# Performance work log

Hardware: AMD Instinct MI355X
Metric: run time of the kernel (lower is better)

Reference implementation:

```python
import jax, jax.numpy as jnp
import numpy as np
import math

B, T, C = 2, 2048, 1024
H = 16
HD = C // H  # 64
LAMBDA_INIT = 0.7 - 0.6 * math.exp(-0.3 * (2 - 1))
EPS = 1e-5


def setup_inputs() -> dict:
    key = jax.random.key(0)
    ks = jax.random.split(key, 12)
    s = 1.0 / math.sqrt(C)
    return {
        'x':   jax.random.normal(ks[0], (B, T, C), jnp.float32),
        'Wq1': jax.random.normal(ks[1], (C, C), jnp.float32) * s,
        'Wq2': jax.random.normal(ks[2], (C, C), jnp.float32) * s,
        'Wk1': jax.random.normal(ks[3], (C, C), jnp.float32) * s,
        'Wk2': jax.random.normal(ks[4], (C, C), jnp.float32) * s,
        'Wv':  jax.random.normal(ks[5], (2 * C, C), jnp.float32) * s,
        'Wc':  jax.random.normal(ks[6], (C, 2 * C), jnp.float32) * (1.0 / math.sqrt(2 * C)),
        'lq1': jax.random.normal(ks[7], (H, HD), jnp.float32) * 0.1,
        'lk1': jax.random.normal(ks[8], (H, HD), jnp.float32) * 0.1,
        'lq2': jax.random.normal(ks[9], (H, HD), jnp.float32) * 0.1,
        'lk2': jax.random.normal(ks[10], (H, HD), jnp.float32) * 0.1,
    }


def _heads(x, W, d):
    # x:[B,T,C] @ W.T:[C,out] -> [B,H,T,d]
    b, t, _ = x.shape
    return jnp.einsum('btc,dc->btd', x, W).reshape(b, t, H, d).transpose(0, 2, 1, 3)


def reference(x, Wq1, Wq2, Wk1, Wk2, Wv, Wc, lq1, lk1, lq2, lk2):
    b, t, c = x.shape
    q1 = _heads(x, Wq1, HD)
    q2 = _heads(x, Wq2, HD)
    k1 = _heads(x, Wk1, HD)
    k2 = _heads(x, Wk2, HD)
    v = _heads(x, Wv, 2 * HD)  # [B,H,T,2hd]
    scale = 1.0 / math.sqrt(HD)
    causal = jnp.tril(jnp.ones((t, t), bool))  # [T,T]
    neg = jnp.float32(-jnp.inf)
    att1 = jnp.einsum('bhqd,bhkd->bhqk', q1, k1) * scale
    att2 = jnp.einsum('bhqd,bhkd->bhqk', q2, k2) * scale
    att1 = jax.nn.softmax(jnp.where(causal, att1, neg), axis=-1)
    att2 = jax.nn.softmax(jnp.where(causal, att2, neg), axis=-1)
    lam1 = jnp.exp(jnp.sum(lq1 * lk1, -1))  # [H]
    lam2 = jnp.exp(jnp.sum(lq2 * lk2, -1))
    lam_full = (lam1 - lam2 + LAMBDA_INIT)[None, :, None, None]
    att = att1 - lam_full * att2
    y = jnp.einsum('bhqk,bhkd->bhqd', att, v)  # [B,H,T,2hd]
    # sub-layernorm over last dim, no affine
    mu = jnp.mean(y, -1, keepdims=True)
    var = jnp.mean(jnp.square(y - mu), -1, keepdims=True)
    y = (y - mu) * jax.lax.rsqrt(var + EPS)
    y = y * (1.0 - LAMBDA_INIT)
    y = y.transpose(0, 2, 1, 3).reshape(b, t, 2 * c)
    return jnp.einsum('btd,cd->btc', y, Wc)
```

## Files before the change

### kernel.cpp

```cpp
#include <hip/hip_runtime.h>
#include <stdint.h>

typedef unsigned short u16;
typedef unsigned int   u32;
typedef short  short8  __attribute__((ext_vector_type(8)));
typedef float  f32x4   __attribute__((ext_vector_type(4)));
typedef u16    u16x4   __attribute__((ext_vector_type(4)));
typedef u32    u32x4   __attribute__((ext_vector_type(4)));

#define LAMBDA_INIT   0.25550906759096927f
#define ONE_MINUS_LI  0.7444909324090307f
#define QSCALE        0.18033688011112043f

__device__ __forceinline__ u16 f2bf(float f) {
  union { float f; u32 u; } v; v.f = f;
  u32 r = v.u + 0x7fffu + ((v.u >> 16) & 1u);
  return (u16)(r >> 16);
}

__device__ __forceinline__ u32 packtr(float a, float b) {
  return (__builtin_bit_cast(u32, a) >> 16) | (__builtin_bit_cast(u32, b) & 0xffff0000u);
}

__device__ __forceinline__ float expv(float x) {
  float r; asm("v_exp_f32 %0, %1" : "=v"(r) : "v"(x)); return r;
}

__device__ __forceinline__ void gload16(const void* g, void* l) {
  __builtin_amdgcn_global_load_lds(
      (const __attribute__((address_space(1))) void*)g,
      (__attribute__((address_space(3))) void*)l, 16, 0, 0);
}

__global__ __launch_bounds__(256) void k_cvt12(
    const float* __restrict__ x,  const float* __restrict__ wq1,
    const float* __restrict__ wq2, const float* __restrict__ wk1,
    const float* __restrict__ wk2, const float* __restrict__ wv,
    const float* __restrict__ wc,
    u16* __restrict__ xb, u16* __restrict__ wall, u16* __restrict__ wcb) {
  const int seg = blockIdx.y;
  const float* s;
  u16* d;
  if (seg < 4)       { s = x + (size_t)seg * 1048576;        d = xb + (size_t)seg * 1048576; }
  else if (seg == 4) { s = wq1;                              d = wall; }
  else if (seg == 5) { s = wq2;                              d = wall + 1048576; }
  else if (seg == 6) { s = wk1;                              d = wall + 2097152; }
  else if (seg == 7) { s = wk2;                              d = wall + 3145728; }
  else if (seg < 10) { s = wv + (size_t)(seg - 8) * 1048576; d = wall + 4194304 + (size_t)(seg - 8) * 1048576; }
  else               { s = wc + (size_t)(seg - 10) * 1048576; d = wcb + (size_t)(seg - 10) * 1048576; }
  int i = (blockIdx.x * 256 + threadIdx.x) * 4;
  float4 v = *(const float4*)(s + i);
  u16x4 o = { f2bf(v.x), f2bf(v.y), f2bf(v.z), f2bf(v.w) };
  *(u16x4*)(d + i) = o;
}

__device__ __forceinline__ void gemm_tile_128(
    const u16* __restrict__ A, const u16* __restrict__ Bm, int K,
    int m0, int n0, char* smem, f32x4 acc[4][4]) {
  const int tid = threadIdx.x;
  const int l = tid & 63, w = tid >> 6, g = l >> 4, q = l & 15;
  const int wm = w >> 1, wn = w & 1;
  char* As = smem;
  char* Bs = smem + 16384;
#pragma unroll
  for (int mi = 0; mi < 4; mi++)
#pragma unroll
    for (int ni = 0; ni < 4; ni++) acc[mi][ni] = (f32x4){0.f, 0.f, 0.f, 0.f};

  const int nkt = K >> 6;
  for (int kt = 0; kt < nkt; ++kt) {
    __syncthreads();
#pragma unroll
    for (int i = 0; i < 4; i++) {
      int cc = i * 256 + tid;
      int row = cc >> 3, off = cc & 7;
      int sw = (off * 16) ^ ((row & 7) << 4);
      gload16((const char*)A + ((size_t)(m0 + row) * K + kt * 64) * 2 + sw, As + cc * 16);
      gload16((const char*)Bm + ((size_t)(n0 + row) * K + kt * 64) * 2 + sw, Bs + cc * 16);
    }
    __syncthreads();
#pragma unroll
    for (int ks = 0; ks < 2; ++ks) {
      short8 af[4], bf[4];
#pragma unroll
      for (int mi = 0; mi < 4; mi++) {
        int row = wm * 64 + mi * 16 + q;
        af[mi] = *(const short8*)(As + ((row * 128 + ks * 64 + g * 16) ^ ((row & 7) << 4)));
      }
#pragma unroll
      for (int ni = 0; ni < 4; ni++) {
        int row = wn * 64 + ni * 16 + q;
        bf[ni] = *(const short8*)(Bs + ((row * 128 + ks * 64 + g * 16) ^ ((row & 7) << 4)));
      }
#pragma unroll
      for (int mi = 0; mi < 4; mi++)
#pragma unroll
        for (int ni = 0; ni < 4; ni++)
          acc[mi][ni] = __builtin_amdgcn_mfma_f32_16x16x32_bf16(af[mi], bf[ni], acc[mi][ni], 0, 0, 0);
    }
  }
}

__global__ __launch_bounds__(256) void k_gemm_qkv(
    const u16* __restrict__ xb, const u16* __restrict__ wall,
    u16* __restrict__ q1, u16* __restrict__ q2,
    u16* __restrict__ k1, u16* __restrict__ k2,
    u16* __restrict__ vt) {
  __shared__ __align__(16) char smem[32768];
  f32x4 acc[4][4];
  const int n0 = blockIdx.x * 128, m0 = blockIdx.y * 128;
  gemm_tile_128(xb, wall, 1024, m0, n0, smem, acc);

  const int l = threadIdx.x & 63, w = threadIdx.x >> 6, g = l >> 4, q = l & 15;
  const int wm = w >> 1, wn = w & 1;
  const int seg = n0 >> 10;
  const float sc = (seg < 2) ? QSCALE : 1.0f;
  u16* qk = (seg == 0) ? q1 : (seg == 1) ? q2 : (seg == 2) ? k1 : k2;
#pragma unroll
  for (int mi = 0; mi < 4; mi++)
#pragma unroll
    for (int ni = 0; ni < 4; ni++) {
      int row0 = m0 + wm * 64 + mi * 16 + 4 * g;
      int col = n0 + wn * 64 + ni * 16 + q;
      int bb = row0 >> 11;
      if (seg < 4) {
        int h = (col >> 6) & 15, hd = col & 63;
#pragma unroll
        for (int r = 0; r < 4; r++) {
          int t = (row0 + r) & 2047;
          qk[(((size_t)bb * 16 + h) * 2048 + t) * 64 + hd] = f2bf(acc[mi][ni][r] * sc);
        }
      } else {
        int nv = col - 4096, hh = nv >> 7, d = nv & 127;
        int t = row0 & 2047;
        u16x4 pv;
#pragma unroll
        for (int r = 0; r < 4; r++) pv[r] = f2bf(acc[mi][ni][r]);
        size_t addr = (size_t)(bb * 16 + hh) * 262144 + (size_t)(t >> 6) * 8192
                    + (size_t)(((((t >> 5) & 1) * 8 + (d >> 4)) * 512)
                               + ((t >> 3) & 3) * 128 + (d & 15) * 8 + (t & 7));
        *(u16x4*)(vt + addr) = pv;
      }
    }
}

__global__ __launch_bounds__(256) void k_attn(
    const u16* __restrict__ q1p, const u16* __restrict__ q2p,
    const u16* __restrict__ k1p, const u16* __restrict__ k2p,
    const u16* __restrict__ vfp,
    const float* __restrict__ lq1, const float* __restrict__ lk1,
    const float* __restrict__ lq2, const float* __restrict__ lk2,
    u16* __restrict__ ybp) {
  __shared__ __align__(16) char smem[32768];
  const int fid = blockIdx.x;
  const int xcd = fid & 7;
  const int p = (fid >> 3) & 31;
  const int k = fid >> 8;
  const int t8 = p >> 2;
  const int tile = (k == 0) ? (31 - t8) : (k == 1) ? t8
                 : (k == 2) ? (23 - t8) : (8 + t8);
  const int bh = xcd * 4 + (p & 3);
  const int b = bh >> 4, h = bh & 15;
  const int tid = threadIdx.x, w = tid >> 6, l = tid & 63, g = l >> 4, q = l & 15;
  const int nchunk = 2 * tile + 2;
  const int qrow = tile * 64 + w * 16 + q;

  float a1 = lq1[h * 64 + l] * lk1[h * 64 + l];
  float a2 = lq2[h * 64 + l] * lk2[h * 64 + l];
#pragma unroll
  for (int off = 32; off; off >>= 1) {
    a1 += __shfl_xor(a1, off);
    a2 += __shfl_xor(a2, off);
  }
  const float lam = expf(a1) - expf(a2) + LAMBDA_INIT;

  short8 qf[2][2];
  {
    size_t qoff = ((size_t)bh * 2048 + qrow) * 64;
#pragma unroll
    for (int ks = 0; ks < 2; ++ks) {
      qf[0][ks] = *(const short8*)(q1p + qoff + ks * 32 + g * 8);
      qf[1][ks] = *(const short8*)(q2p + qoff + ks * 32 + g * 8);
    }
  }
  f32x4 o[2][8];
  float lsum[2] = {0.f, 0.f};
#pragma unroll
  for (int s = 0; s < 2; s++)
#pragma unroll
    for (int mt = 0; mt < 8; mt++) o[s][mt] = (f32x4){0.f, 0.f, 0.f, 0.f};

  auto stage_kv = [&](char* sb, int kv0) {
    int kv = tid >> 3, off = tid & 7;
    int sw = (off * 16) ^ ((kv & 7) << 4);
    size_t rb = ((size_t)bh * 2048 + kv0 + kv) * 128;
    gload16((const char*)k1p + rb + sw, sb + tid * 16);
    gload16((const char*)k2p + rb + sw, sb + 4096 + tid * 16);
    const char* vsrc = (const char*)vfp + (size_t)bh * 524288
                     + (size_t)(kv0 >> 6) * 16384 + (size_t)((kv0 >> 5) & 1) * 8192;
    gload16(vsrc + tid * 16, sb + 8192 + tid * 16);
    gload16(vsrc + 4096 + tid * 16, sb + 12288 + tid * 16);
  };

  stage_kv(smem, 0);

  for (int i = 0; i < nchunk; ++i) {
    char* sb = smem + (i & 1) * 16384;
    asm volatile("s_waitcnt vmcnt(0)" ::: "memory");
    __builtin_amdgcn_s_barrier();
    if (i + 1 < nchunk) stage_kv(smem + ((i + 1) & 1) * 16384, (i + 1) * 32);

    const int kv0 = i * 32;
    const bool diag = (i >= nchunk - 2);

    u32 pk[2][4];
#pragma unroll
    for (int s = 0; s < 2; ++s) {
      const char* Ks = sb + s * 4096;
      f32x4 s0 = {0.f, 0.f, 0.f, 0.f}, s1 = {0.f, 0.f, 0.f, 0.f};
#pragma unroll
      for (int ks = 0; ks < 2; ++ks) {
        short8 af0 = *(const short8*)(Ks + ((q * 128 + ks * 64 + g * 16) ^ ((q & 7) << 4)));
        short8 af1 = *(const short8*)(Ks + (((16 + q) * 128 + ks * 64 + g * 16) ^ ((q & 7) << 4)));
        s0 = __builtin_amdgcn_mfma_f32_16x16x32_bf16(af0, qf[s][ks], s0, 0, 0, 0);
        s1 = __builtin_amdgcn_mfma_f32_16x16x32_bf16(af1, qf[s][ks], s1, 0, 0, 0);
      }
      const int kb0 = kv0 + 4 * g, kb1 = kb0 + 16;
      if (diag) {
#pragma unroll
        for (int r = 0; r < 4; r++) {
          s0[r] = (kb0 + r > qrow) ? -1e30f : s0[r];
          s1[r] = (kb1 + r > qrow) ? -1e30f : s1[r];
        }
      }
      float p0[4], p1[4], rs = 0.f;
#pragma unroll
      for (int r = 0; r < 4; r++) {
        p0[r] = expv(s0[r]);
        p1[r] = expv(s1[r]);
        rs += p0[r] + p1[r];
      }
      lsum[s] += rs;

      u32 pk0[2] = { packtr(p0[0], p0[1]), packtr(p0[2], p0[3]) };
      u32 pk1[2] = { packtr(p1[0], p1[1]), packtr(p1[2], p1[3]) };
      int srcA = q + (g & 1) * 32;
      int srcB = srcA + 16;
      u32 xa0 = (u32)__shfl((int)pk0[0], srcA), xa1 = (u32)__shfl((int)pk0[1], srcA);
      u32 xa2 = (u32)__shfl((int)pk0[0], srcB), xa3 = (u32)__shfl((int)pk0[1], srcB);
      u32 xb0 = (u32)__shfl((int)pk1[0], srcA), xb1 = (u32)__shfl((int)pk1[1], srcA);
      u32 xb2 = (u32)__shfl((int)pk1[0], srcB), xb3 = (u32)__shfl((int)pk1[1], srcB);
      bool lo = (g < 2);
      pk[s][0] = lo ? xa0 : xb0;
      pk[s][1] = lo ? xa1 : xb1;
      pk[s][2] = lo ? xa2 : xb2;
      pk[s][3] = lo ? xa3 : xb3;
    }
    u32x4 t0 = {pk[0][0], pk[0][1], pk[0][2], pk[0][3]};
    u32x4 t1 = {pk[1][0], pk[1][1], pk[1][2], pk[1][3]};
    short8 pf0 = __builtin_bit_cast(short8, t0);
    short8 pf1 = __builtin_bit_cast(short8, t1);
    const char* Vb = sb + 8192 + l * 16;
    __builtin_amdgcn_s_setprio(1);
#pragma unroll
    for (int mt = 0; mt < 8; ++mt) {
      short8 vf = *(const short8*)(Vb + mt * 1024);
      o[0][mt] = __builtin_amdgcn_mfma_f32_16x16x32_bf16(vf, pf0, o[0][mt], 0, 0, 0);
      o[1][mt] = __builtin_amdgcn_mfma_f32_16x16x32_bf16(vf, pf1, o[1][mt], 0, 0, 0);
    }
    __builtin_amdgcn_s_setprio(0);
  }

  float l0 = lsum[0]; l0 += __shfl_xor(l0, 16); l0 += __shfl_xor(l0, 32);
  float l1 = lsum[1]; l1 += __shfl_xor(l1, 16); l1 += __shfl_xor(l1, 32);
  const float inv0 = 1.f / l0, inv1 = 1.f / l1;
  float sum = 0.f, ssq = 0.f;
#pragma unroll
  for (int mt = 0; mt < 8; ++mt)
#pragma unroll
    for (int r = 0; r < 4; r++) {
      float y = o[0][mt][r] * inv0 - lam * (o[1][mt][r] * inv1);
      o[0][mt][r] = y;
      sum += y;
      ssq += y * y;
    }
  sum += __shfl_xor(sum, 16); sum += __shfl_xor(sum, 32);
  ssq += __shfl_xor(ssq, 16); ssq += __shfl_xor(ssq, 32);
  const float mean = sum * (1.f / 128.f);
  const float var = ssq * (1.f / 128.f) - mean * mean;
  const float rstd = rsqrtf(var + 1e-5f) * ONE_MINUS_LI;
  u16* dst = ybp + ((size_t)(b * 2048 + qrow)) * 2048 + h * 128;
#pragma unroll
  for (int mt = 0; mt < 8; ++mt) {
    u16x4 pv;
#pragma unroll
    for (int r = 0; r < 4; r++) pv[r] = f2bf((o[0][mt][r] - mean) * rstd);
    *(u16x4*)(dst + mt * 16 + 4 * g) = pv;
  }
}

__global__ __launch_bounds__(512) void k_gemm_out(
    const u16* __restrict__ yb, const u16* __restrict__ wcb,
    float* __restrict__ out) {
  __shared__ __align__(16) char smem[32768];
  const int tid = threadIdx.x;
  const int l = tid & 63, w = tid >> 6, g = l >> 4, q = l & 15;
  const int wm = w >> 1, wn = w & 1;
  const int n0 = blockIdx.x * 128, m0 = blockIdx.y * 128;
  char* As = smem;
  char* Bs = smem + 16384;
  f32x4 acc[2][4];
#pragma unroll
  for (int mi = 0; mi < 2; mi++)
#pragma unroll
    for (int ni = 0; ni < 4; ni++) acc[mi][ni] = (f32x4){0.f, 0.f, 0.f, 0.f};

  for (int kt = 0; kt < 32; ++kt) {
    __syncthreads();
#pragma unroll
    for (int i = 0; i < 2; i++) {
      int cc = i * 512 + tid;
      int row = cc >> 3, off = cc & 7;
      int sw = (off * 16) ^ ((row & 7) << 4);
      gload16((const char*)yb + ((size_t)(m0 + row) * 2048 + kt * 64) * 2 + sw, As + cc * 16);
      gload16((const char*)wcb + ((size_t)(n0 + row) * 2048 + kt * 64) * 2 + sw, Bs + cc * 16);
    }
    __syncthreads();
#pragma unroll
    for (int ks = 0; ks < 2; ++ks) {
      short8 af[2], bf[4];
#pragma unroll
      for (int mi = 0; mi < 2; mi++) {
        int row = wm * 32 + mi * 16 + q;
        af[mi] = *(const short8*)(As + ((row * 128 + ks * 64 + g * 16) ^ ((row & 7) << 4)));
      }
#pragma unroll
      for (int ni = 0; ni < 4; ni++) {
        int row = wn * 64 + ni * 16 + q;
        bf[ni] = *(const short8*)(Bs + ((row * 128 + ks * 64 + g * 16) ^ ((row & 7) << 4)));
      }
#pragma unroll
      for (int mi = 0; mi < 2; mi++)
#pragma unroll
        for (int ni = 0; ni < 4; ni++)
          acc[mi][ni] = __builtin_amdgcn_mfma_f32_16x16x32_bf16(af[mi], bf[ni], acc[mi][ni], 0, 0, 0);
    }
  }
#pragma unroll
  for (int mi = 0; mi < 2; mi++)
#pragma unroll
    for (int ni = 0; ni < 4; ni++)
#pragma unroll
      for (int r = 0; r < 4; r++) {
        int row = m0 + wm * 32 + mi * 16 + 4 * g + r;
        int col = n0 + wn * 64 + ni * 16 + q;
        out[(size_t)row * 1024 + col] = acc[mi][ni][r];
      }
}

extern "C" void kernel_launch(void* const* d_in, const int* in_sizes, int n_in,
                              void* d_out, int out_size, void* d_ws, size_t ws_size,
                              hipStream_t stream) {
  const float* x   = (const float*)d_in[0];
  const float* Wq1 = (const float*)d_in[1];
  const float* Wq2 = (const float*)d_in[2];
  const float* Wk1 = (const float*)d_in[3];
  const float* Wk2 = (const float*)d_in[4];
  const float* Wv  = (const float*)d_in[5];
  const float* Wc  = (const float*)d_in[6];
  const float* lq1 = (const float*)d_in[7];
  const float* lk1 = (const float*)d_in[8];
  const float* lq2 = (const float*)d_in[9];
  const float* lk2 = (const float*)d_in[10];

  char* ws = (char*)d_ws;
  u16* xb   = (u16*)(ws);
  u16* wall = (u16*)(ws + 8388608);
  u16* wcb  = (u16*)(ws + 20971520);
  u16* q1   = (u16*)(ws + 25165824);
  u16* q2   = (u16*)(ws + 33554432);
  u16* k1   = (u16*)(ws + 41943040);
  u16* k2   = (u16*)(ws + 50331648);
  u16* vt   = (u16*)(ws + 58720256);
  u16* yb   = (u16*)(ws + 75497472);

  k_cvt12<<<dim3(1024, 12), 256, 0, stream>>>(x, Wq1, Wq2, Wk1, Wk2, Wv, Wc,
                                              xb, wall, wcb);
  k_gemm_qkv<<<dim3(48, 32), 256, 0, stream>>>(xb, wall, q1, q2, k1, k2, vt);
  k_attn<<<1024, 256, 0, stream>>>(q1, q2, k1, k2, vt,
                                   lq1, lk1, lq2, lk2, yb);
  k_gemm_out<<<dim3(8, 32), 512, 0, stream>>>(yb, wcb, (float*)d_out);
}
```

Before: 197.9 us.

## Double-buffer LDS tiles in QKV and output GEMMs to overlap loads with MFMA

Both projection GEMMs now keep two 32KB shared-memory stages, issuing the global-to-LDS loads for tile k+1 right after the barrier and then computing on tile k. This replaces the two-barrier load-then-compute loop and is meant to hide global memory latency behind MFMA work. It doubles LDS use to 64KB per block, which can lower occupancy. Correctness also depends on the vmcnt wait plus a single barrier being enough to protect the reused buffer.

```diff
diff --git a/kernel.cpp b/kernel.cpp
--- a/kernel.cpp
+++ b/kernel.cpp
@@ -54,65 +54,61 @@
   *(u16x4*)(d + i) = o;
 }
 
-__device__ __forceinline__ void gemm_tile_128(
-    const u16* __restrict__ A, const u16* __restrict__ Bm, int K,
-    int m0, int n0, char* smem, f32x4 acc[4][4]) {
-  const int tid = threadIdx.x;
-  const int l = tid & 63, w = tid >> 6, g = l >> 4, q = l & 15;
-  const int wm = w >> 1, wn = w & 1;
-  char* As = smem;
-  char* Bs = smem + 16384;
-#pragma unroll
-  for (int mi = 0; mi < 4; mi++)
-#pragma unroll
-    for (int ni = 0; ni < 4; ni++) acc[mi][ni] = (f32x4){0.f, 0.f, 0.f, 0.f};
-
-  const int nkt = K >> 6;
-  for (int kt = 0; kt < nkt; ++kt) {
-    __syncthreads();
-#pragma unroll
-    for (int i = 0; i < 4; i++) {
-      int cc = i * 256 + tid;
-      int row = cc >> 3, off = cc & 7;
-      int sw = (off * 16) ^ ((row & 7) << 4);
-      gload16((const char*)A + ((size_t)(m0 + row) * K + kt * 64) * 2 + sw, As + cc * 16);
-      gload16((const char*)Bm + ((size_t)(n0 + row) * K + kt * 64) * 2 + sw, Bs + cc * 16);
-    }
-    __syncthreads();
-#pragma unroll
-    for (int ks = 0; ks < 2; ++ks) {
-      short8 af[4], bf[4];
-#pragma unroll
-      for (int mi = 0; mi < 4; mi++) {
-        int row = wm * 64 + mi * 16 + q;
-        af[mi] = *(const short8*)(As + ((row * 128 + ks * 64 + g * 16) ^ ((row & 7) << 4)));
-      }
-#pragma unroll
-      for (int ni = 0; ni < 4; ni++) {
-        int row = wn * 64 + ni * 16 + q;
-        bf[ni] = *(const short8*)(Bs + ((row * 128 + ks * 64 + g * 16) ^ ((row & 7) << 4)));
-      }
-#pragma unroll
-      for (int mi = 0; mi < 4; mi++)
-#pragma unroll
-        for (int ni = 0; ni < 4; ni++)
-          acc[mi][ni] = __builtin_amdgcn_mfma_f32_16x16x32_bf16(af[mi], bf[ni], acc[mi][ni], 0, 0, 0);
-    }
-  }
-}
-
 __global__ __launch_bounds__(256) void k_gemm_qkv(
     const u16* __restrict__ xb, const u16* __restrict__ wall,
     u16* __restrict__ q1, u16* __restrict__ q2,
     u16* __restrict__ k1, u16* __restrict__ k2,
     u16* __restrict__ vt) {
-  __shared__ __align__(16) char smem[32768];
+  __shared__ __align__(16) char smem[65536];
+  const int tid = threadIdx.x;
+  const int l = tid & 63, w = tid >> 6, g = l >> 4, q = l & 15;
+  const int wm = w >> 1, wn = w & 1;
+  const int n0 = blockIdx.x * 128, m0 = blockIdx.y * 128;
   f32x4 acc[4][4];
-  const int n0 = blockIdx.x * 128, m0 = blockIdx.y * 128;
-  gemm_tile_128(xb, wall, 1024, m0, n0, smem, acc);
-
-  const int l = threadIdx.x & 63, w = threadIdx.x >> 6, g = l >> 4, q = l & 15;
-  const int wm = w >> 1, wn = w & 1;
+#pragma unroll
+  for (int mi = 0; mi < 4; mi++)
+#pragma unroll
+    for (int ni = 0; ni < 4; ni++) acc[mi][ni] = (f32x4){0.f, 0.f, 0.f, 0.f};
+
+  auto stage = [&](char* sb, int kt) {
+#pragma unroll
+    for (int i = 0; i < 4; i++) {
+      int cc = i * 256 + tid;
+      int row = cc >> 3, off = cc & 7;
+      int sw = (off * 16) ^ ((row & 7) << 4);
+      gload16((const char*)xb + ((size_t)(m0 + row) * 1024 + kt * 64) * 2 + sw, sb + cc * 16);
+      gload16((const char*)wall + ((size_t)(n0 + row) * 1024 + kt * 64) * 2 + sw, sb + 16384 + cc * 16);
+    }
+  };
+
+  stage(smem, 0);
+  for (int kt = 0; kt < 16; ++kt) {
+    asm volatile("s_waitcnt vmcnt(0)" ::: "memory");
+    __builtin_amdgcn_s_barrier();
+    if (kt + 1 < 16) stage(smem + ((kt + 1) & 1) * 32768, kt + 1);
+    const char* As = smem + (kt & 1) * 32768;
+    const char* Bs = As + 16384;
+#pragma unroll
+    for (int ks = 0; ks < 2; ++ks) {
+      short8 af[4], bf[4];
+#pragma unroll
+      for (int mi = 0; mi < 4; mi++) {
+        int row = wm * 64 + mi * 16 + q;
+        af[mi] = *(const short8*)(As + ((row * 128 + ks * 64 + g * 16) ^ ((row & 7) << 4)));
+      }
+#pragma unroll
+      for (int ni = 0; ni < 4; ni++) {
+        int row = wn * 64 + ni * 16 + q;
+        bf[ni] = *(const short8*)(Bs + ((row * 128 + ks * 64 + g * 16) ^ ((row & 7) << 4)));
+      }
+#pragma unroll
+      for (int mi = 0; mi < 4; mi++)
+#pragma unroll
+        for (int ni = 0; ni < 4; ni++)
+          acc[mi][ni] = __builtin_amdgcn_mfma_f32_16x16x32_bf16(af[mi], bf[ni], acc[mi][ni], 0, 0, 0);
+    }
+  }
+
   const int seg = n0 >> 10;
   const float sc = (seg < 2) ? QSCALE : 1.0f;
   u16* qk = (seg == 0) ? q1 : (seg == 1) ? q2 : (seg == 2) ? k1 : k2;
@@ -302,30 +298,35 @@
 __global__ __launch_bounds__(512) void k_gemm_out(
     const u16* __restrict__ yb, const u16* __restrict__ wcb,
     float* __restrict__ out) {
-  __shared__ __align__(16) char smem[32768];
+  __shared__ __align__(16) char smem[65536];
   const int tid = threadIdx.x;
   const int l = tid & 63, w = tid >> 6, g = l >> 4, q = l & 15;
   const int wm = w >> 1, wn = w & 1;
   const int n0 = blockIdx.x * 128, m0 = blockIdx.y * 128;
-  char* As = smem;
-  char* Bs = smem + 16384;
   f32x4 acc[2][4];
 #pragma unroll
   for (int mi = 0; mi < 2; mi++)
 #pragma unroll
     for (int ni = 0; ni < 4; ni++) acc[mi][ni] = (f32x4){0.f, 0.f, 0.f, 0.f};
 
-  for (int kt = 0; kt < 32; ++kt) {
-    __syncthreads();
+  auto stage = [&](char* sb, int kt) {
 #pragma unroll
     for (int i = 0; i < 2; i++) {
       int cc = i * 512 + tid;
       int row = cc >> 3, off = cc & 7;
       int sw = (off * 16) ^ ((row & 7) << 4);
-      gload16((const char*)yb + ((size_t)(m0 + row) * 2048 + kt * 64) * 2 + sw, As + cc * 16);
-      gload16((const char*)wcb + ((size_t)(n0 + row) * 2048 + kt * 64) * 2 + sw, Bs + cc * 16);
-    }
-    __syncthreads();
+      gload16((const char*)yb + ((size_t)(m0 + row) * 2048 + kt * 64) * 2 + sw, sb + cc * 16);
+      gload16((const char*)wcb + ((size_t)(n0 + row) * 2048 + kt * 64) * 2 + sw, sb + 16384 + cc * 16);
+    }
+  };
+
+  stage(smem, 0);
+  for (int kt = 0; kt < 32; ++kt) {
+    asm volatile("s_waitcnt vmcnt(0)" ::: "memory");
+    __builtin_amdgcn_s_barrier();
+    if (kt + 1 < 32) stage(smem + ((kt + 1) & 1) * 32768, kt + 1);
+    const char* As = smem + (kt & 1) * 32768;
+    const char* Bs = As + 16384;
 #pragma unroll
     for (int ks = 0; ks < 2; ++ks) {
       short8 af[2], bf[4];
```

New measurement: 189.7 us, median of 2. 1.04x faster.
